# Kernel optimization log

Hardware: AMD Instinct MI355X
Metric: run time of the kernel (lower is better)

Reference implementation:

```python
import jax, jax.numpy as jnp
import numpy as np

N, H, W, DIM = 8, 32, 32, 768
HEAD_DIM = 64
NUM_HEADS = DIM // HEAD_DIM
KERNEL = (7, 7)
ROT_DIM = HEAD_DIM // 2  # 32
POS_DIM = 2
THETA = 10000.0
LN_EPS = 1e-5


def setup_inputs() -> dict:
    key = jax.random.key(0)
    k_x, k_qkv, k_out = jax.random.split(key, 3)
    S = H * W
    x = jax.random.normal(k_x, (N, S, DIM), dtype=jnp.float32)
    # 2D grid positions, same for every batch element
    grid = jnp.stack(jnp.meshgrid(jnp.arange(H), jnp.arange(W), indexing='ij'), axis=-1)
    pos = jnp.broadcast_to(grid.reshape(1, S, 2), (N, S, 2)).astype(jnp.int32)
    padding_mask = jnp.ones((N, S), dtype=bool)
    ln_g = jnp.ones((DIM,), dtype=jnp.float32)
    ln_b = jnp.zeros((DIM,), dtype=jnp.float32)
    w_qkv = jax.random.normal(k_qkv, (DIM, 3 * DIM), dtype=jnp.float32) * 0.02
    b_qkv = jnp.zeros((3 * DIM,), dtype=jnp.float32)
    w_out = jax.random.normal(k_out, (DIM, DIM), dtype=jnp.float32) * 0.02
    b_out = jnp.zeros((DIM,), dtype=jnp.float32)
    return {"x": x, "pos": pos, "padding_mask": padding_mask,
            "ln_g": ln_g, "ln_b": ln_b,
            "w_qkv": w_qkv, "b_qkv": b_qkv,
            "w_out": w_out, "b_out": b_out}


def _rope_cos_sin(pos):
    # freqs: theta ** linspace(0, -1, rot_dim // (pos_dim*2) + 1)[:-1] -> 8 freqs
    n_freq = ROT_DIM // (POS_DIM * 2)
    freqs = THETA ** jnp.linspace(0.0, -1.0, n_freq + 1, dtype=jnp.float32)[:-1]
    # pos: [n, s, 2] -> [n, s, 2, n_freq] -> [n, s, 2*n_freq] -> [n, 1, s, 2*n_freq]
    tmp = (pos[..., None].astype(jnp.float32) * freqs).reshape(*pos.shape[:-1], -1)[:, None]
    return jnp.cos(tmp), jnp.sin(tmp)


def _apply_rotary(x, cos, sin):
    d = cos.shape[-1]  # 16
    x1, x2, x3 = x[..., :d], x[..., d:2 * d], x[..., 2 * d:]
    y1 = x1 * cos - x2 * sin
    y2 = x2 * cos + x1 * sin
    return jnp.concatenate((y1.astype(x3.dtype), y2.astype(x3.dtype), x3), axis=-1)


def _attn_mask(pos, padding_mask, kernel_size):
    dh = pos[:, :, None, 0] - pos[:, None, :, 0]  # [n, s, s]
    dw = pos[:, :, None, 1] - pos[:, None, :, 1]
    kh, kw = kernel_size
    m = ((dh <= kh // 2) & (dh > -((kh + 1) // 2))
         & (dw <= kw // 2) & (dw > -((kw + 1) // 2)))
    m = m & (padding_mask[:, None, :] & padding_mask[:, :, None])
    return m[:, None]  # [n, 1, s, s]


def reference(x, pos, padding_mask, ln_g, ln_b, w_qkv, b_qkv, w_out, b_out):
    n, s, dim = x.shape
    skip = x
    # LayerNorm
    mu = jnp.mean(x, axis=-1, keepdims=True)
    var = jnp.mean(jnp.square(x - mu), axis=-1, keepdims=True)
    xn = (x - mu) * jax.lax.rsqrt(var + LN_EPS) * ln_g + ln_b
    # QKV projection; split 'n s (t h d)'
    qkv = xn @ w_qkv + b_qkv                       # [n, s, 3*dim]
    qkv = qkv.reshape(n, s, 3, NUM_HEADS, HEAD_DIM)
    qkv = jnp.transpose(qkv, (2, 0, 3, 1, 4))      # [3, n, h, s, d]
    q, k, v = qkv[0], qkv[1], qkv[2]
    # RoPE on first half of head dim
    cos, sin = _rope_cos_sin(pos)
    q = _apply_rotary(q, cos, sin)
    k = _apply_rotary(k, cos, sin)
    # Local 2D-window masked SDPA
    mask = _attn_mask(pos, padding_mask, KERNEL)   # [n, 1, s, s]
    scale = 1.0 / jnp.sqrt(jnp.asarray(HEAD_DIM, dtype=q.dtype))
    scores = jnp.einsum('nhqd,nhkd->nhqk', q, k) * scale
    scores = jnp.where(mask, scores, jnp.asarray(-1e30, dtype=scores.dtype))
    attn = jax.nn.softmax(scores, axis=-1)
    o = jnp.einsum('nhqk,nhkd->nhqd', attn, v)     # [n, h, s, d]
    o = jnp.transpose(o, (0, 2, 1, 3)).reshape(n, s, dim)
    return o @ w_out + b_out + skip
```

## Files before the change

kernel.cpp:

```cpp
#include <hip/hip_runtime.h>


typedef unsigned short u16;
typedef unsigned int   u32;
typedef __attribute__((ext_vector_type(8))) short v8s;
typedef __attribute__((ext_vector_type(4))) float v4f;
typedef __attribute__((ext_vector_type(4))) unsigned short v4us;

#define MFMA16(a,b,c) __builtin_amdgcn_mfma_f32_16x16x32_bf16((a),(b),(c),0,0,0)

__device__ __forceinline__ u16 f2bf(float f){
  union { float f; u32 u; } v; v.f = f;
  u32 u = v.u;
  u32 r = u + 0x7FFFu + ((u >> 16) & 1u);
  return (u16)(r >> 16);
}
__device__ __forceinline__ float bf2f(u16 h){
  union { u32 u; float f; } v; v.u = ((u32)h) << 16;
  return v.f;
}
__device__ __forceinline__ void gll16(const void* g, void* l){
  __builtin_amdgcn_global_load_lds((const __attribute__((address_space(1))) void*)g,
                                   (__attribute__((address_space(3))) void*)l, 16, 0, 0);
}
__device__ __forceinline__ v8s ld8(const u16* p){ return *(const v8s*)p; }
__device__ __forceinline__ void st8(u16* p, v8s v){ *(v8s*)p = v; }

__global__ __launch_bounds__(256)
void jet_prep(const float* __restrict__ x, const float* __restrict__ g,
              const float* __restrict__ b, u16* __restrict__ xn,
              const float* __restrict__ w0, u16* __restrict__ t0,
              const float* __restrict__ w1, u16* __restrict__ t1)
{
  __shared__ float sh[32 * 33];
  const int bid = blockIdx.x, t = threadIdx.x;
  if (bid < 8192){
    const float* xr = x + (size_t)bid * 768;
    float a0 = xr[t], a1 = xr[t + 256], a2 = xr[t + 512];
    float s  = a0 + a1 + a2;
    float ss = a0*a0 + a1*a1 + a2*a2;
    #pragma unroll
    for (int o = 1; o < 64; o <<= 1){ s += __shfl_xor(s, o); ss += __shfl_xor(ss, o); }
    const int wv = t >> 6, lane = t & 63;
    if (lane == 0){ sh[wv] = s; sh[4 + wv] = ss; }
    __syncthreads();
    s  = sh[0] + sh[1] + sh[2] + sh[3];
    ss = sh[4] + sh[5] + sh[6] + sh[7];
    const float mu = s * (1.0f / 768.0f);
    const float var = ss * (1.0f / 768.0f) - mu * mu;
    const float rs = rsqrtf(var + 1e-5f);
    u16* o = xn + (size_t)bid * 768;
    o[t]       = f2bf((a0 - mu) * rs * g[t]       + b[t]);
    o[t + 256] = f2bf((a1 - mu) * rs * g[t + 256] + b[t + 256]);
    o[t + 512] = f2bf((a2 - mu) * rs * g[t + 512] + b[t + 512]);
  } else {
    const float* in; u16* out; int C, bx, by;
    if (bid < 8192 + 1728){
      const int tb = bid - 8192; in = w0; out = t0; C = 2304; bx = tb % 72; by = tb / 72;
    } else {
      const int tb = bid - 8192 - 1728; in = w1; out = t1; C = 768; bx = tb % 24; by = tb / 24;
    }
    float (*tile)[33] = (float(*)[33])sh;
    const int x0 = bx << 5, y0 = by << 5;
    const int tx = t & 31, ty = t >> 5;
    #pragma unroll
    for (int i = 0; i < 32; i += 8)
      tile[ty + i][tx] = in[(size_t)(y0 + ty + i) * C + x0 + tx];
    __syncthreads();
    #pragma unroll
    for (int i = 0; i < 32; i += 8)
      out[(size_t)(x0 + ty + i) * 768 + y0 + tx] = f2bf(tile[tx][ty + i]);
  }
}

template<int MODE>
__global__ __launch_bounds__(256, 4)
void jet_gemm(const u16* __restrict__ A, const u16* __restrict__ Bt,
              const float* __restrict__ bias, int K,
              u16* __restrict__ qbuf, u16* __restrict__ kbuf, u16* __restrict__ vbuf,
              const float* __restrict__ skip, float* __restrict__ outp)
{
  __shared__ u16 As[2][128 * 32];
  __shared__ u16 Bs[2][128 * 32];
  const int tid = threadIdx.x;
  const int lane = tid & 63, wv = tid >> 6;
  const int wm = wv >> 1, wn = wv & 1;
  const int row0 = blockIdx.x * 128, col0 = blockIdx.y * 128;
  const int lq = lane & 15, lk = lane >> 4;

  v4f acc[4][4] = {};

  auto stage = [&](int bsel, int kt){
    const int k0 = kt * 32;
    #pragma unroll
    for (int i = 0; i < 2; ++i){
      const int lin = i * 256 + tid;
      const int r = lin >> 2, c = lin & 3;
      const int sc = c ^ ((r >> 1) & 3);
      gll16(A  + (size_t)(row0 + r) * K + k0 + (sc << 3), (void*)&As[bsel][lin << 3]);
      gll16(Bt + (size_t)(col0 + r) * K + k0 + (sc << 3), (void*)&Bs[bsel][lin << 3]);
    }
  };

  stage(0, 0);
  __syncthreads();
  const int KT = K >> 5;
  for (int kt = 0; kt < KT; ++kt){
    const int cur = kt & 1;
    if (kt + 1 < KT) stage(cur ^ 1, kt + 1);
    v8s af[4], bf[4];
    #pragma unroll
    for (int m = 0; m < 4; ++m){
      const int row_ = wm*64 + m*16 + lq;
      af[m] = ld8(&As[cur][row_*32 + ((lk ^ ((row_ >> 1) & 3)) << 3)]);
    }
    #pragma unroll
    for (int n = 0; n < 4; ++n){
      const int row_ = wn*64 + n*16 + lq;
      bf[n] = ld8(&Bs[cur][row_*32 + ((lk ^ ((row_ >> 1) & 3)) << 3)]);
    }
    #pragma unroll
    for (int m = 0; m < 4; ++m)
      #pragma unroll
      for (int n = 0; n < 4; ++n)
        acc[m][n] = MFMA16(af[m], bf[n], acc[m][n]);
    __syncthreads();
  }

  if (MODE == 0){
    const int colw = col0 + wn * 64;
    const int which = colw / 768;
    const int cm = colw - which * 768;
    const int hh = cm >> 6;
    float bb[4];
    #pragma unroll
    for (int n = 0; n < 4; ++n) bb[n] = bias[colw + n * 16 + lq];

    if (which == 2){
      #pragma unroll
      for (int m = 0; m < 4; ++m){
        const int rbase = row0 + wm * 64 + m * 16 + lk * 4;
        const int img = rbase >> 10, s = rbase & 1023;
        u16* vp = vbuf + (size_t)(img * 12 + hh) * 64 * 1024;
        #pragma unroll
        for (int n = 0; n < 4; ++n){
          const int d = n * 16 + lq;
          v4us pk;
          #pragma unroll
          for (int r = 0; r < 4; ++r) pk[r] = f2bf(acc[m][n][r] + bb[n]);
          *(v4us*)&vp[(size_t)d * 1024 + s] = pk;
        }
      }
    } else {
      u16* dst0 = (which == 0) ? qbuf : kbuf;
      const float freq = __expf(-(float)(lq & 7) * 1.1512925464970229f);
      #pragma unroll
      for (int m = 0; m < 4; ++m){
        const int rbase = row0 + wm * 64 + m * 16 + lk * 4;
        const int img = rbase >> 10, sb = rbase & 1023;
        u16* dst = dst0 + ((size_t)(img * 12 + hh) * 1024 + sb) * 64;
        #pragma unroll
        for (int r = 0; r < 4; ++r){
          const int s = sb + r;
          const float coord = (float)((lq < 8) ? (s >> 5) : (s & 31));
          float sn, cs;
          __sincosf(coord * freq, &sn, &cs);
          const float x1 = acc[m][0][r] + bb[0];
          const float x2 = acc[m][1][r] + bb[1];
          u16* dr = dst + (size_t)r * 64;
          dr[lq]      = f2bf(x1 * cs - x2 * sn);
          dr[16 + lq] = f2bf(x2 * cs + x1 * sn);
          dr[32 + lq] = f2bf(acc[m][2][r] + bb[2]);
          dr[48 + lq] = f2bf(acc[m][3][r] + bb[3]);
        }
      }
    }
  } else {
    #pragma unroll
    for (int m = 0; m < 4; ++m){
      const int rbase = row0 + wm*64 + m*16 + lk*4;
      #pragma unroll
      for (int n = 0; n < 4; ++n){
        const int col = col0 + wn*64 + n*16 + lq;
        const float bb = bias[col];
        const size_t o = (size_t)rbase * 768 + col;
        #pragma unroll
        for (int r = 0; r < 4; ++r)
          outp[o + (size_t)r * 768] = acc[m][n][r] + bb + skip[o + (size_t)r * 768];
      }
    }
  }
}

__global__ __launch_bounds__(64, 2)
void jet_attn(const u16* __restrict__ qbuf, const u16* __restrict__ kbuf,
              const u16* __restrict__ vbuf, u16* __restrict__ obuf)
{
  __shared__ u16 Ps[32][232];

  const int b0 = blockIdx.x;
  const int blk = (b0 & 7) * 384 + (b0 >> 3);
  const int qh = blk & 31;
  const int nh = blk >> 5;
  const int img = nh / 12, hd = nh - img * 12;
  int h0 = qh - 3; h0 = h0 < 0 ? 0 : (h0 > 25 ? 25 : h0);
  const int s0k = h0 * 32;
  const int lane = threadIdx.x;
  const int lq = lane & 15, lk = lane >> 4;

  const u16* kg = kbuf + ((size_t)nh * 1024 + s0k) * 64;
  const u16* vg = vbuf + (size_t)nh * 64 * 1024;

  const u16* qrow0 = qbuf + ((size_t)nh * 1024 + qh * 32 + lq) * 64;
  const u16* qrow1 = qrow0 + 16 * 64;
  const v8s qa0 = ld8(qrow0 + lk * 8), qa1 = ld8(qrow0 + 32 + lk * 8);
  const v8s qb0 = ld8(qrow1 + lk * 8), qb1 = ld8(qrow1 + 32 + lk * 8);

  float sa[56], sb[56];
  #pragma unroll
  for (int tt = 0; tt < 14; ++tt){
    const u16* krow = kg + (size_t)(tt * 16 + lq) * 64;
    const v8s kf0 = ld8(krow + lk * 8);
    const v8s kf1 = ld8(krow + 32 + lk * 8);
    v4f s0 = {0.f, 0.f, 0.f, 0.f}, s1 = {0.f, 0.f, 0.f, 0.f};
    s0 = MFMA16(kf0, qa0, s0); s0 = MFMA16(kf1, qa1, s0);
    s1 = MFMA16(kf0, qb0, s1); s1 = MFMA16(kf1, qb1, s1);
    #pragma unroll
    for (int r = 0; r < 4; ++r){
      const int k = tt * 16 + lk * 4 + r;
      const int dh = qh - (h0 + (k >> 5));
      const int kw = k & 31;
      const bool okh = (dh <= 3) & (dh >= -3);
      const int dwa = lq - kw, dwb = 16 + lq - kw;
      sa[tt * 4 + r] = (okh & (dwa <= 3) & (dwa >= -3)) ? s0[r] * 0.125f : -1e30f;
      sb[tt * 4 + r] = (okh & (dwb <= 3) & (dwb >= -3)) ? s1[r] * 0.125f : -1e30f;
    }
  }

  float mxa = -1e30f, mxb = -1e30f;
  #pragma unroll
  for (int i = 0; i < 56; ++i){ mxa = fmaxf(mxa, sa[i]); mxb = fmaxf(mxb, sb[i]); }
  mxa = fmaxf(mxa, __shfl_xor(mxa, 16)); mxa = fmaxf(mxa, __shfl_xor(mxa, 32));
  mxb = fmaxf(mxb, __shfl_xor(mxb, 16)); mxb = fmaxf(mxb, __shfl_xor(mxb, 32));
  float suma = 0.f, sumb = 0.f;
  #pragma unroll
  for (int i = 0; i < 56; ++i){
    const float ea = __expf(sa[i] - mxa); sa[i] = ea; suma += ea;
    const float eb = __expf(sb[i] - mxb); sb[i] = eb; sumb += eb;
  }
  suma += __shfl_xor(suma, 16); suma += __shfl_xor(suma, 32);
  sumb += __shfl_xor(sumb, 16); sumb += __shfl_xor(sumb, 32);
  const float inva = 1.0f / suma, invb = 1.0f / sumb;

  #pragma unroll
  for (int tt = 0; tt < 14; ++tt){
    v4us pka, pkb;
    #pragma unroll
    for (int r = 0; r < 4; ++r){
      pka[r] = f2bf(sa[tt * 4 + r] * inva);
      pkb[r] = f2bf(sb[tt * 4 + r] * invb);
    }
    *(v4us*)&Ps[lq][tt * 16 + lk * 4]      = pka;
    *(v4us*)&Ps[16 + lq][tt * 16 + lk * 4] = pkb;
  }

  v4f accA[4] = {}, accB[4] = {};
  #pragma unroll
  for (int ks = 0; ks < 7; ++ks){
    const v8s pa = ld8(&Ps[lq][ks * 32 + lk * 8]);
    const v8s pb = ld8(&Ps[16 + lq][ks * 32 + lk * 8]);
    #pragma unroll
    for (int n = 0; n < 4; ++n){
      const v8s vf = ld8(vg + (size_t)(n * 16 + lq) * 1024 + s0k + ks * 32 + lk * 8);
      accA[n] = MFMA16(pa, vf, accA[n]);
      accB[n] = MFMA16(pb, vf, accB[n]);
    }
  }

  u16* dst = obuf + ((size_t)img * 1024 + qh * 32) * 768 + hd * 64;
  #pragma unroll
  for (int n = 0; n < 4; ++n)
    #pragma unroll
    for (int r = 0; r < 4; ++r){
      dst[(size_t)(lk * 4 + r) * 768 + n * 16 + lq]      = f2bf(accA[n][r]);
      dst[(size_t)(16 + lk * 4 + r) * 768 + n * 16 + lq] = f2bf(accB[n][r]);
    }
}

extern "C" void kernel_launch(void* const* d_in, const int* in_sizes, int n_in,
                              void* d_out, int out_size, void* d_ws, size_t ws_size,
                              hipStream_t stream)
{
  const float* x     = (const float*)d_in[0];
  const float* ln_g  = (const float*)d_in[3];
  const float* ln_b  = (const float*)d_in[4];
  const float* w_qkv = (const float*)d_in[5];
  const float* b_qkv = (const float*)d_in[6];
  const float* w_out = (const float*)d_in[7];
  const float* b_out = (const float*)d_in[8];
  float* out = (float*)d_out;

  char* ws = (char*)d_ws;
  size_t off = 0;
  auto alloc = [&](size_t n){ size_t o = off; off += (n + 255) & ~(size_t)255; return o; };
  u16* xn    = (u16*)(ws + alloc(8192ull * 768 * 2));
  u16* wqkvT = (u16*)(ws + alloc(2304ull * 768 * 2));
  u16* woutT = (u16*)(ws + alloc(768ull  * 768 * 2));
  u16* q_buf = (u16*)(ws + alloc(96ull * 1024 * 64 * 2));
  u16* k_buf = (u16*)(ws + alloc(96ull * 1024 * 64 * 2));
  u16* v_buf = (u16*)(ws + alloc(96ull * 1024 * 64 * 2));
  u16* o_buf = (u16*)(ws + alloc(8192ull * 768 * 2));

  jet_prep<<<8192 + 1728 + 576, 256, 0, stream>>>(x, ln_g, ln_b, xn, w_qkv, wqkvT, w_out, woutT);
  jet_gemm<0><<<dim3(64, 18), 256, 0, stream>>>(xn, wqkvT, b_qkv, 768,
                                                q_buf, k_buf, v_buf, nullptr, nullptr);
  jet_attn<<<3072, 64, 0, stream>>>(q_buf, k_buf, v_buf, o_buf);
  jet_gemm<1><<<dim3(64, 6), 256, 0, stream>>>(o_buf, woutT, b_out, 768,
                                               nullptr, nullptr, nullptr, x, out);
}
```

Baseline: 113.3 us.

## Load GEMM A operand directly from global into registers, bypassing LDS

The A tile is no longer staged through shared memory. Each wave loads its own A fragments straight from global memory into registers, double-buffered across two K-steps, while B keeps its LDS double buffer. The aim is to cut LDS traffic and footprint and remove the A LDS reads. In exchange it uses more registers (occupancy hint lowered from 4 to 3), the per-lane global loads are less coalesced, and A rows are re-fetched by both waves that share a row.

New measurement: 145.3 us. 1.28x slower.

```diff
diff --git a/kernel.cpp b/kernel.cpp
--- a/kernel.cpp
+++ b/kernel.cpp
@@ -74,13 +74,12 @@
 }
 
 template<int MODE>
-__global__ __launch_bounds__(256, 4)
+__global__ __launch_bounds__(256, 3)
 void jet_gemm(const u16* __restrict__ A, const u16* __restrict__ Bt,
               const float* __restrict__ bias, int K,
               u16* __restrict__ qbuf, u16* __restrict__ kbuf, u16* __restrict__ vbuf,
               const float* __restrict__ skip, float* __restrict__ outp)
 {
-  __shared__ u16 As[2][128 * 32];
   __shared__ u16 Bs[2][128 * 32];
   const int tid = threadIdx.x;
   const int lane = tid & 63, wv = tid >> 6;
@@ -90,42 +89,56 @@
 
   v4f acc[4][4] = {};
 
-  auto stage = [&](int bsel, int kt){
+  auto stageB = [&](int bsel, int kt){
     const int k0 = kt * 32;
     #pragma unroll
     for (int i = 0; i < 2; ++i){
       const int lin = i * 256 + tid;
       const int r = lin >> 2, c = lin & 3;
       const int sc = c ^ ((r >> 1) & 3);
-      gll16(A  + (size_t)(row0 + r) * K + k0 + (sc << 3), (void*)&As[bsel][lin << 3]);
       gll16(Bt + (size_t)(col0 + r) * K + k0 + (sc << 3), (void*)&Bs[bsel][lin << 3]);
     }
   };
 
-  stage(0, 0);
+  #define LDB(bf, bsel) { _Pragma("unroll") for (int n = 0; n < 4; ++n){ \
+      const int row_ = wn*64 + n*16 + lq; \
+      bf[n] = ld8(&Bs[bsel][row_*32 + ((lk ^ ((row_ >> 1) & 3)) << 3)]); }}
+  #define MM(aset, bf) { _Pragma("unroll") for (int m = 0; m < 4; ++m) \
+      _Pragma("unroll") for (int n = 0; n < 4; ++n) \
+        acc[m][n] = MFMA16(aset[m], bf[n], acc[m][n]); }
+
+  const u16* pa[4];
+  #pragma unroll
+  for (int m = 0; m < 4; ++m)
+    pa[m] = A + (size_t)(row0 + wm*64 + m*16 + lq) * K + lk*8;
+
+  v8s aA[4], aB[4], bf[4];
+  #pragma unroll
+  for (int m = 0; m < 4; ++m) aA[m] = ld8(pa[m]);
+  stageB(0, 0);
   __syncthreads();
+
   const int KT = K >> 5;
-  for (int kt = 0; kt < KT; ++kt){
-    const int cur = kt & 1;
-    if (kt + 1 < KT) stage(cur ^ 1, kt + 1);
-    v8s af[4], bf[4];
-    #pragma unroll
-    for (int m = 0; m < 4; ++m){
-      const int row_ = wm*64 + m*16 + lq;
-      af[m] = ld8(&As[cur][row_*32 + ((lk ^ ((row_ >> 1) & 3)) << 3)]);
-    }
-    #pragma unroll
-    for (int n = 0; n < 4; ++n){
-      const int row_ = wn*64 + n*16 + lq;
-      bf[n] = ld8(&Bs[cur][row_*32 + ((lk ^ ((row_ >> 1) & 3)) << 3)]);
-    }
-    #pragma unroll
-    for (int m = 0; m < 4; ++m)
-      #pragma unroll
-      for (int n = 0; n < 4; ++n)
-        acc[m][n] = MFMA16(af[m], bf[n], acc[m][n]);
+  for (int kt = 0; kt < KT; kt += 2){
+    if (kt + 1 < KT){
+      stageB(1, kt + 1);
+      #pragma unroll
+      for (int m = 0; m < 4; ++m) aB[m] = ld8(pa[m] + 32);
+    }
+    LDB(bf, 0); MM(aA, bf);
     __syncthreads();
-  }
+    if (kt + 2 < KT){
+      stageB(0, kt + 2);
+      #pragma unroll
+      for (int m = 0; m < 4; ++m) aA[m] = ld8(pa[m] + 64);
+    }
+    LDB(bf, 1); MM(aB, bf);
+    __syncthreads();
+    #pragma unroll
+    for (int m = 0; m < 4; ++m) pa[m] += 64;
+  }
+  #undef LDB
+  #undef MM
 
   if (MODE == 0){
     const int colw = col0 + wn * 64;
```
